# Performance work log

Measured on AMD Instinct MI355X. Metric: run time of the kernel, lower is better.

Reference implementation:

```python
import jax, jax.numpy as jnp
import numpy as np

NUM_HEADS = 8
NUM_LEVELS = 4
NUM_POINTS = 4


def setup_inputs() -> dict:
    key = jax.random.key(0)
    kq, kp, kv, k1, k2, k3, k4 = jax.random.split(key, 7)
    B, Q, C = 4, 4096, 256
    M, L, P = NUM_HEADS, NUM_LEVELS, NUM_POINTS
    shapes_np = np.array([[128, 128], [64, 64], [32, 32], [16, 16]], dtype=np.int32)
    sizes = shapes_np[:, 0] * shapes_np[:, 1]
    N = int(sizes.sum())  # 21760
    level_index = jnp.asarray(np.concatenate([[0], np.cumsum(sizes)[:-1]]).astype(np.int32))
    q = jax.random.normal(kq, (B, Q, C), jnp.float32)
    p = jax.random.uniform(kp, (B, Q, L, 2), jnp.float32)  # normalized ref points
    v = jax.random.normal(kv, (B, N, C), jnp.float32)
    # proj_offset bias: radial grid init from reset_parameters()
    t = np.arange(M, dtype=np.float32) * (2.0 * np.pi / M)
    grid = np.stack([np.cos(t), np.sin(t)], -1)
    grid = grid / np.abs(grid).max(-1, keepdims=True)
    grid = np.tile(grid[:, None, None, :], (1, L, P, 1)) * np.arange(1, P + 1, dtype=np.float32)[None, None, :, None]
    b_off = jnp.asarray(grid.reshape(-1))
    s = 1.0 / np.sqrt(C).astype(np.float32)
    W_off = jax.random.normal(k1, (C, M * L * P * 2), jnp.float32) * 0.01
    W_attn = jax.random.normal(k2, (C, M * L * P), jnp.float32) * s
    b_attn = jnp.zeros((M * L * P,), jnp.float32)
    W_val = jax.random.normal(k3, (C, C), jnp.float32) * s
    b_val = jnp.zeros((C,), jnp.float32)
    W_out = jax.random.normal(k4, (C, C), jnp.float32) * s
    b_out = jnp.zeros((C,), jnp.float32)
    return {"q": q, "p": p, "v": v, "shapes": jnp.asarray(shapes_np), "level_index": level_index,
            "W_off": W_off, "b_off": b_off, "W_attn": W_attn, "b_attn": b_attn,
            "W_val": W_val, "b_val": b_val, "W_out": W_out, "b_out": b_out}


def _ms_deform_attn(q, p, v, shapes, level_index, W_off, b_off, W_attn, b_attn, W_val, b_val, W_out, b_out):
    B, Q, C = q.shape
    M, L, P = NUM_HEADS, NUM_LEVELS, NUM_POINTS
    D = C // M
    N = v.shape[1]
    # value projection -> [B, M, N, D] (head-major for gather)
    v_p = (v @ W_val + b_val).reshape(B, N, M, D).transpose(0, 2, 1, 3)
    # attention weights, softmax over L*P (classic MSDeformAttn kernel contract)
    attn = jax.nn.softmax((q @ W_attn + b_attn).reshape(B, Q, M, L * P), axis=-1)
    attn = attn.reshape(B, Q, M, L, P)
    # sampling locations (P==2 reference-point branch)
    off = (q @ W_off + b_off).reshape(B, Q, M, L, P, 2)
    norm = jnp.stack([shapes[:, 1], shapes[:, 0]], -1).astype(jnp.float32)  # (W, H) per level
    loc = p[:, :, None, :, None, :] + off / norm[None, None, None, :, None, :]  # [B,Q,M,L,P,2]

    out = jnp.zeros((B, M, Q, D), jnp.float32)
    for l in range(L):
        Hf = shapes[l, 0].astype(jnp.float32)
        Wf = shapes[l, 1].astype(jnp.float32)
        Hi = shapes[l, 0]
        Wi = shapes[l, 1]
        base = level_index[l]
        # grid_sample(align_corners=False) convention: pixel = loc*size - 0.5
        x = loc[:, :, :, l, :, 0] * Wf - 0.5  # [B,Q,M,P]
        y = loc[:, :, :, l, :, 1] * Hf - 0.5
        x0 = jnp.floor(x)
        y0 = jnp.floor(y)
        lx, ly = x - x0, y - y0
        x0i = x0.astype(jnp.int32)
        y0i = y0.astype(jnp.int32)

        def corner(xi, yi, w):
            valid = (xi >= 0) & (xi < Wi) & (yi >= 0) & (yi < Hi)
            idx = base + jnp.clip(yi, 0, Hi - 1) * Wi + jnp.clip(xi, 0, Wi - 1)  # [B,Q,M,P]
            idx = idx.transpose(0, 2, 1, 3).reshape(B, M, Q * P)
            g = jnp.take_along_axis(v_p, idx[..., None], axis=2).reshape(B, M, Q, P, D)
            wv = (w * valid.astype(w.dtype)).transpose(0, 2, 1, 3)[..., None]  # [B,M,Q,P,1]
            return g * wv

        samp = (corner(x0i, y0i, (1 - lx) * (1 - ly))
                + corner(x0i + 1, y0i, lx * (1 - ly))
                + corner(x0i, y0i + 1, (1 - lx) * ly)
                + corner(x0i + 1, y0i + 1, lx * ly))  # [B,M,Q,P,D]
        a_l = attn[:, :, :, l, :].transpose(0, 2, 1, 3)  # [B,M,Q,P]
        out = out + jnp.einsum('bmqpd,bmqp->bmqd', samp, a_l)

    out = out.transpose(0, 2, 1, 3).reshape(B, Q, M * D)
    return out @ W_out + b_out


def reference(q, p, v, shapes, level_index, W_off, b_off, W_attn, b_attn, W_val, b_val, W_out, b_out):
    return _ms_deform_attn(q, p, v, shapes, level_index, W_off, b_off, W_attn, b_attn, W_val, b_val, W_out, b_out)
```

## Files before the change

### kernel.cpp

```cpp
#include <hip/hip_runtime.h>
#include <cstddef>

#define BB 4
#define QQ 4096
#define MM 8
#define NN 21760

typedef __bf16 bf16_8 __attribute__((ext_vector_type(8)));
typedef __bf16 bf16_4 __attribute__((ext_vector_type(4)));
typedef float  floatx4 __attribute__((ext_vector_type(4)));

__global__ __launch_bounds__(256) void prep_weights(
    const float* __restrict__ Wv, const float* __restrict__ Wa,
    const float* __restrict__ Wo, const float* __restrict__ Wu,
    const float* __restrict__ ba, const float* __restrict__ bo,
    __bf16* __restrict__ Wt, float* __restrict__ biasq)
{
    const int gid = blockIdx.x * 256 + threadIdx.x;
    if (gid < 65536) {
        const int n = gid >> 8, k = gid & 255;
        Wt[gid] = (__bf16)Wv[k * 256 + n];
    } else if (gid < 163840) {
        const int o = gid - 65536;
        const int n = o >> 8, k = o & 255;
        Wt[gid] = (__bf16)(n < 128 ? Wa[k * 128 + n] : Wo[k * 256 + (n - 128)]);
    } else if (gid < 229376) {
        const int o = gid - 163840;
        const int n = o >> 8, k = o & 255;
        Wt[gid] = (__bf16)Wu[k * 256 + n];
    } else if (gid < 229760) {
        const int j = gid - 229376;
        biasq[j] = (j < 128) ? ba[j] : bo[j - 128];
    }
}

template<typename AT, int NCB, int MODE>
__global__ __launch_bounds__(512, 4) void gemm_ws(
    const AT* __restrict__ A,
    const __bf16* __restrict__ Wn,
    const float* __restrict__ bias,
    void* __restrict__ Cout,
    int tokens, int ldc)
{
    constexpr int F  = NCB / 8;
    constexpr int NJ = F / 16;

    const int z    = blockIdx.z;
    const int col0 = blockIdx.x * NCB;
    const AT* Ab   = A + (size_t)z * tokens * 256;
    const __bf16* Wb = Wn + (size_t)col0 * 256;

    __shared__ __bf16 As[64][256];

    const int tid  = threadIdx.x;
    const int lane = tid & 63;
    const int wave = tid >> 6;
    const int quad = lane >> 4;
    const int l16  = lane & 15;
    const int wave_f = wave * F;

    bf16_8 wf[8][NJ];
    #pragma unroll
    for (int kk = 0; kk < 8; ++kk)
        #pragma unroll
        for (int j = 0; j < NJ; ++j)
            wf[kk][j] = *(const bf16_8*)(Wb + (size_t)(wave_f + j * 16 + l16) * 256
                                          + kk * 32 + quad * 8);

    const int token0 = blockIdx.y * 64;
    if (sizeof(AT) == 4) {
        const float* Af = (const float*)Ab;
        #pragma unroll
        for (int c = 0; c < 8; ++c) {
            const int cid = c * 512 + tid;
            const int r   = cid >> 6;
            const int kc  = (cid & 63) * 4;
            const float4 av = *(const float4*)(Af + (size_t)(token0 + r) * 256 + kc);
            bf16_4 w;
            w[0] = (__bf16)av.x; w[1] = (__bf16)av.y;
            w[2] = (__bf16)av.z; w[3] = (__bf16)av.w;
            const int col = ((((kc >> 3) ^ (r & 7)) << 3) | (kc & 7));
            *(bf16_4*)&As[r][col] = w;
        }
    } else {
        const __bf16* Ah = (const __bf16*)Ab;
        #pragma unroll
        for (int c = 0; c < 4; ++c) {
            const int cid = c * 512 + tid;
            const int r   = cid >> 5;
            const int kc  = (cid & 31) * 8;
            const bf16_8 av = *(const bf16_8*)(Ah + (size_t)(token0 + r) * 256 + kc);
            const int col = (((kc >> 3) ^ (r & 7)) << 3);
            *(bf16_8*)&As[r][col] = av;
        }
    }
    __syncthreads();

    floatx4 acc[NJ][4] = {};
    #pragma unroll
    for (int kk = 0; kk < 8; ++kk) {
        bf16_8 af[4];
        #pragma unroll
        for (int it = 0; it < 4; ++it)
            af[it] = *(const bf16_8*)&As[it * 16 + l16]
                                       [(((kk * 4 + quad) ^ (l16 & 7)) << 3)];
        #pragma unroll
        for (int j = 0; j < NJ; ++j)
            #pragma unroll
            for (int it = 0; it < 4; ++it)
                acc[j][it] = __builtin_amdgcn_mfma_f32_16x16x32_bf16(wf[kk][j], af[it], acc[j][it], 0, 0, 0);
    }

    #pragma unroll
    for (int j = 0; j < NJ; ++j) {
        const int n0 = col0 + wave_f + j * 16 + quad * 4;
        const float4 b4 = *(const float4*)(bias + n0);
        #pragma unroll
        for (int it = 0; it < 4; ++it) {
            const int token = token0 + it * 16 + l16;
            const float v0 = acc[j][it][0] + b4.x;
            const float v1 = acc[j][it][1] + b4.y;
            const float v2 = acc[j][it][2] + b4.z;
            const float v3 = acc[j][it][3] + b4.w;
            if (MODE == 0) {
                float4 o; o.x = v0; o.y = v1; o.z = v2; o.w = v3;
                *(float4*)((float*)Cout + ((size_t)z * tokens + token) * ldc + n0) = o;
            } else {
                const int mh = n0 >> 5, dd = n0 & 31;
                bf16_4 ob;
                ob[0] = (__bf16)v0; ob[1] = (__bf16)v1; ob[2] = (__bf16)v2; ob[3] = (__bf16)v3;
                *(bf16_4*)((__bf16*)Cout + (((size_t)z * 8 + mh) * NN + token) * 32 + dd) = ob;
            }
        }
    }
}

__device__ __forceinline__ float bflo(unsigned u) { return __uint_as_float(u << 16); }
__device__ __forceinline__ float bfhi(unsigned u) { return __uint_as_float(u & 0xffff0000u); }

__global__ __launch_bounds__(512) void sampler(
    const __bf16* __restrict__ vp,
    const float* __restrict__ gqp,
    const float* __restrict__ pref,
    __bf16* __restrict__ mid)
{
    const int t    = threadIdx.x;
    const int m    = t >> 6;
    const int lane = t & 63;
    const int s    = lane >> 2;
    const int c    = lane & 3;
    const int l    = s >> 2;
    const int bq   = blockIdx.x;
    const int b    = bq >> 12;

    const int   Hi = 128 >> l;
    const float Hf = (float)Hi;
    const int   base = (l == 0) ? 0 : (l == 1) ? 16384 : (l == 2) ? 20480 : 21504;

    const float logit = gqp[(size_t)bq * 384 + m * 16 + s];
    const float e = __expf(logit);
    float sum = e;
    #pragma unroll
    for (int k = 4; k < 64; k <<= 1) sum += __shfl_xor(sum, k, 64);
    const float a = e * __builtin_amdgcn_rcpf(sum);

    const float2 off = *(const float2*)(gqp + (size_t)bq * 384 + 128 + (m * 16 + s) * 2);
    const float2 pr  = *(const float2*)(pref + (size_t)bq * 8 + l * 2);

    const float x = fmaf(pr.x, Hf, off.x - 0.5f);
    const float y = fmaf(pr.y, Hf, off.y - 0.5f);
    const float x0f = floorf(x), y0f = floorf(y);
    const float lx = x - x0f, ly = y - y0f;
    const int x0 = (int)x0f, y0 = (int)y0f;
    const int cx0 = min(max(x0, 0), Hi - 1), cx1 = min(max(x0 + 1, 0), Hi - 1);
    const int cy0 = min(max(y0, 0), Hi - 1), cy1 = min(max(y0 + 1, 0), Hi - 1);
    const bool vx0 = (x0 >= 0) && (x0 < Hi), vx1 = (x0 + 1 >= 0) && (x0 + 1 < Hi);
    const bool vy0 = (y0 >= 0) && (y0 < Hi), vy1 = (y0 + 1 >= 0) && (y0 + 1 < Hi);
    const float w00 = a * (1.f - lx) * (1.f - ly) * ((vx0 && vy0) ? 1.f : 0.f);
    const float w10 = a * lx * (1.f - ly) * ((vx1 && vy0) ? 1.f : 0.f);
    const float w01 = a * (1.f - lx) * ly * ((vx0 && vy1) ? 1.f : 0.f);
    const float w11 = a * lx * ly * ((vx1 && vy1) ? 1.f : 0.f);

    const __bf16* vbase = vp + ((size_t)b * 8 + m) * NN * 32;
    const uint4 u00 = *((const uint4*)(vbase + (size_t)(base + cy0 * Hi + cx0) * 32) + c);
    const uint4 u10 = *((const uint4*)(vbase + (size_t)(base + cy0 * Hi + cx1) * 32) + c);
    const uint4 u01 = *((const uint4*)(vbase + (size_t)(base + cy1 * Hi + cx0) * 32) + c);
    const uint4 u11 = *((const uint4*)(vbase + (size_t)(base + cy1 * Hi + cx1) * 32) + c);

    float f[8];
    f[0] = w00*bflo(u00.x) + w10*bflo(u10.x) + w01*bflo(u01.x) + w11*bflo(u11.x);
    f[1] = w00*bfhi(u00.x) + w10*bfhi(u10.x) + w01*bfhi(u01.x) + w11*bfhi(u11.x);
    f[2] = w00*bflo(u00.y) + w10*bflo(u10.y) + w01*bflo(u01.y) + w11*bflo(u11.y);
    f[3] = w00*bfhi(u00.y) + w10*bfhi(u10.y) + w01*bfhi(u01.y) + w11*bfhi(u11.y);
    f[4] = w00*bflo(u00.z) + w10*bflo(u10.z) + w01*bflo(u01.z) + w11*bflo(u11.z);
    f[5] = w00*bfhi(u00.z) + w10*bfhi(u10.z) + w01*bfhi(u01.z) + w11*bfhi(u11.z);
    f[6] = w00*bflo(u00.w) + w10*bflo(u10.w) + w01*bflo(u01.w) + w11*bflo(u11.w);
    f[7] = w00*bfhi(u00.w) + w10*bfhi(u10.w) + w01*bfhi(u01.w) + w11*bfhi(u11.w);

    const int b2 = (lane >> 2) & 1, b3 = (lane >> 3) & 1, b4i = (lane >> 4) & 1;
    #pragma unroll
    for (int j = 0; j < 4; ++j) {
        const float sel  = b2 ? f[j] : f[j + 4];
        const float recv = __shfl_xor(sel, 4, 64);
        f[j] = (b2 ? f[j + 4] : f[j]) + recv;
    }
    #pragma unroll
    for (int j = 0; j < 2; ++j) {
        const float sel  = b3 ? f[j] : f[j + 2];
        const float recv = __shfl_xor(sel, 8, 64);
        f[j] = (b3 ? f[j + 2] : f[j]) + recv;
    }
    {
        const float sel  = b4i ? f[0] : f[1];
        const float recv = __shfl_xor(sel, 16, 64);
        f[0] = (b4i ? f[1] : f[0]) + recv;
    }
    f[0] += __shfl_xor(f[0], 32, 64);

    if (!(lane & 32)) {
        const int chan = (c << 3) | (b2 << 2) | (b3 << 1) | b4i;
        mid[(size_t)bq * 256 + m * 32 + chan] = (__bf16)f[0];
    }
}

extern "C" void kernel_launch(void* const* d_in, const int* in_sizes, int n_in,
                              void* d_out, int out_size, void* d_ws, size_t ws_size,
                              hipStream_t stream) {
    const float* q      = (const float*)d_in[0];
    const float* p      = (const float*)d_in[1];
    const float* v      = (const float*)d_in[2];
    const float* W_off  = (const float*)d_in[5];
    const float* b_off  = (const float*)d_in[6];
    const float* W_attn = (const float*)d_in[7];
    const float* b_attn = (const float*)d_in[8];
    const float* W_val  = (const float*)d_in[9];
    const float* b_val  = (const float*)d_in[10];
    const float* W_out  = (const float*)d_in[11];
    const float* b_out  = (const float*)d_in[12];
    float* out = (float*)d_out;

    float*  gqp   = (float*)d_ws;
    float*  biasq = gqp + (size_t)16384 * 384;
    __bf16* mid   = (__bf16*)(biasq + 384);
    __bf16* vpb   = mid + (size_t)16384 * 256;
    __bf16* Wt    = vpb + (size_t)BB * 8 * NN * 32;
    __bf16* Wt_val = Wt;
    __bf16* Wt_q   = Wt + 65536;
    __bf16* Wt_out = Wt + 163840;

    prep_weights<<<898, 256, 0, stream>>>(W_val, W_attn, W_off, W_out, b_attn, b_off, Wt, biasq);

    {
        dim3 grid(1, 340, BB);
        gemm_ws<float, 256, 1><<<grid, 512, 0, stream>>>(v, Wt_val, b_val, vpb, NN, 0);
    }
    {
        dim3 grid(3, 256, 1);
        gemm_ws<float, 128, 0><<<grid, 512, 0, stream>>>(q, Wt_q, biasq, gqp, BB * QQ, 384);
    }
    sampler<<<BB * QQ, 512, 0, stream>>>(vpb, gqp, p, mid);
    {
        dim3 grid(2, 256, 1);
        gemm_ws<__bf16, 128, 0><<<grid, 512, 0, stream>>>(mid, Wt_out, b_out, out, BB * QQ, 256);
    }
}
```

Baseline: 246.6 us.

## Fuse value and query projection GEMMs into one launch with async LDS loads

Replaces the separate value-projection and query-projection GEMM launches with a single kernel whose flat block index selects the q or v work. Each block handles 32 tokens and stages fp32 activations directly into LDS via global_load_lds, converting to bf16 at fragment load time. The remaining gemm_ws now issues its weight-fragment loads after the A-tile loads. The intent is to cut a launch, improve load balance and overlap global loads, at the cost of smaller tiles, which reload weights more often per token, and twice as much LDS per row for fp32 staging.

```diff
diff --git a/kernel.cpp b/kernel.cpp
--- a/kernel.cpp
+++ b/kernel.cpp
@@ -34,6 +34,128 @@
     }
 }
 
+__global__ __launch_bounds__(512, 4) void gemm_vq2(
+    const float* __restrict__ v,
+    const float* __restrict__ q,
+    const __bf16* __restrict__ Wt,
+    const float* __restrict__ b_val,
+    const float* __restrict__ biasq,
+    __bf16* __restrict__ vpb,
+    float* __restrict__ gqp)
+{
+    __shared__ float Asf[32][256];
+
+    const int tid  = threadIdx.x;
+    const int lane = tid & 63;
+    const int wave = tid >> 6;
+    const int quad = lane >> 4;
+    const int l16  = lane & 15;
+    const int flat = blockIdx.x;
+
+    const float* Arow;
+    const __bf16* Wpan;
+    int tok0, colbase, z = 0;
+    bool is_vp, two;
+    if (flat < 512) {
+        Arow = q;  Wpan = Wt + 65536;
+        tok0 = flat * 32;  colbase = wave * 32;
+        is_vp = false;  two = true;
+    } else if (flat < 1024) {
+        Arow = q;  Wpan = Wt + 65536;
+        tok0 = (flat - 512) * 32;  colbase = 256 + wave * 16;
+        is_vp = false;  two = false;
+    } else {
+        const int f2 = flat - 1024;
+        z = f2 / 680;
+        tok0 = (f2 - z * 680) * 32;
+        Arow = v + (size_t)z * NN * 256;  Wpan = Wt;
+        colbase = wave * 32;
+        is_vp = true;  two = true;
+    }
+
+    #pragma unroll
+    for (int j = 0; j < 4; ++j) {
+        const int r = wave * 4 + j;
+        const float* gp = Arow + (size_t)(tok0 + r) * 256 + ((lane ^ (r & 7)) << 2);
+        __builtin_amdgcn_global_load_lds(
+            (const __attribute__((address_space(1))) void*)gp,
+            (__attribute__((address_space(3))) void*)&Asf[r][0],
+            16, 0, 0);
+    }
+
+    bf16_8 wf[8][2];
+    #pragma unroll
+    for (int kk = 0; kk < 8; ++kk) {
+        wf[kk][0] = *(const bf16_8*)(Wpan + (size_t)(colbase + l16) * 256 + kk * 32 + quad * 8);
+        if (two)
+            wf[kk][1] = *(const bf16_8*)(Wpan + (size_t)(colbase + 16 + l16) * 256 + kk * 32 + quad * 8);
+    }
+
+    __syncthreads();
+
+    floatx4 acc[2][2] = {};
+    #pragma unroll
+    for (int kk = 0; kk < 8; ++kk) {
+        bf16_8 af[2];
+        #pragma unroll
+        for (int it = 0; it < 2; ++it) {
+            const int rr = it * 16 + l16;
+            const int sw = rr & 7;
+            const int c0 = kk * 8 + quad * 2;
+            const float4 x0 = *(const float4*)&Asf[rr][((c0 ^ sw) << 2)];
+            const float4 x1 = *(const float4*)&Asf[rr][(((c0 + 1) ^ sw) << 2)];
+            bf16_8 t;
+            t[0] = (__bf16)x0.x; t[1] = (__bf16)x0.y;
+            t[2] = (__bf16)x0.z; t[3] = (__bf16)x0.w;
+            t[4] = (__bf16)x1.x; t[5] = (__bf16)x1.y;
+            t[6] = (__bf16)x1.z; t[7] = (__bf16)x1.w;
+            af[it] = t;
+        }
+        #pragma unroll
+        for (int it = 0; it < 2; ++it) {
+            acc[0][it] = __builtin_amdgcn_mfma_f32_16x16x32_bf16(wf[kk][0], af[it], acc[0][it], 0, 0, 0);
+            if (two)
+                acc[1][it] = __builtin_amdgcn_mfma_f32_16x16x32_bf16(wf[kk][1], af[it], acc[1][it], 0, 0, 0);
+        }
+    }
+
+    if (is_vp) {
+        #pragma unroll
+        for (int j = 0; j < 2; ++j) {
+            const int n0 = colbase + j * 16 + quad * 4;
+            const float4 b4 = *(const float4*)(b_val + n0);
+            const int mh = n0 >> 5, dd = n0 & 31;
+            #pragma unroll
+            for (int it = 0; it < 2; ++it) {
+                const int token = tok0 + it * 16 + l16;
+                bf16_4 ob;
+                ob[0] = (__bf16)(acc[j][it][0] + b4.x);
+                ob[1] = (__bf16)(acc[j][it][1] + b4.y);
+                ob[2] = (__bf16)(acc[j][it][2] + b4.z);
+                ob[3] = (__bf16)(acc[j][it][3] + b4.w);
+                *(bf16_4*)(vpb + (((size_t)z * 8 + mh) * NN + token) * 32 + dd) = ob;
+            }
+        }
+    } else {
+        #pragma unroll
+        for (int j = 0; j < 2; ++j) {
+            if (j == 1 && !two) break;
+            const int n0 = colbase + j * 16 + quad * 4;
+            const float4 b4 = *(const float4*)(biasq + n0);
+            #pragma unroll
+            for (int it = 0; it < 2; ++it) {
+                const int token = tok0 + it * 16 + l16;
+                float4 ot;
+                ot.x = acc[j][it][0] + b4.x;
+                ot.y = acc[j][it][1] + b4.y;
+                ot.z = acc[j][it][2] + b4.z;
+                ot.w = acc[j][it][3] + b4.w;
+                *(float4*)(gqp + (size_t)token * 384 + n0) = ot;
+            }
+        }
+    }
+}
+
 template<typename AT, int NCB, int MODE>
 __global__ __launch_bounds__(512, 4) void gemm_ws(
     const AT* __restrict__ A,
@@ -59,14 +181,6 @@
     const int l16  = lane & 15;
     const int wave_f = wave * F;
 
-    bf16_8 wf[8][NJ];
-    #pragma unroll
-    for (int kk = 0; kk < 8; ++kk)
-        #pragma unroll
-        for (int j = 0; j < NJ; ++j)
-            wf[kk][j] = *(const bf16_8*)(Wb + (size_t)(wave_f + j * 16 + l16) * 256
-                                          + kk * 32 + quad * 8);
-
     const int token0 = blockIdx.y * 64;
     if (sizeof(AT) == 4) {
         const float* Af = (const float*)Ab;
@@ -94,6 +208,14 @@
             *(bf16_8*)&As[r][col] = av;
         }
     }
+
+    bf16_8 wf[8][NJ];
+    #pragma unroll
+    for (int kk = 0; kk < 8; ++kk)
+        #pragma unroll
+        for (int j = 0; j < NJ; ++j)
+            wf[kk][j] = *(const bf16_8*)(Wb + (size_t)(wave_f + j * 16 + l16) * 256
+                                          + kk * 32 + quad * 8);
     __syncthreads();
 
     floatx4 acc[NJ][4] = {};
@@ -244,21 +366,14 @@
     __bf16* mid   = (__bf16*)(biasq + 384);
     __bf16* vpb   = mid + (size_t)16384 * 256;
     __bf16* Wt    = vpb + (size_t)BB * 8 * NN * 32;
-    __bf16* Wt_val = Wt;
-    __bf16* Wt_q   = Wt + 65536;
     __bf16* Wt_out = Wt + 163840;
 
     prep_weights<<<898, 256, 0, stream>>>(W_val, W_attn, W_off, W_out, b_attn, b_off, Wt, biasq);
 
-    {
-        dim3 grid(1, 340, BB);
-        gemm_ws<float, 256, 1><<<grid, 512, 0, stream>>>(v, Wt_val, b_val, vpb, NN, 0);
-    }
-    {
-        dim3 grid(3, 256, 1);
-        gemm_ws<float, 128, 0><<<grid, 512, 0, stream>>>(q, Wt_q, biasq, gqp, BB * QQ, 384);
-    }
+    gemm_vq2<<<3744, 512, 0, stream>>>(v, q, Wt, b_val, biasq, vpb, gqp);
+
     sampler<<<BB * QQ, 512, 0, stream>>>(vpb, gqp, p, mid);
+
     {
         dim3 grid(2, 256, 1);
         gemm_ws<__bf16, 128, 0><<<grid, 512, 0, stream>>>(mid, Wt_out, b_out, out, BB * QQ, 256);
```

Result: slower. 266.2 us (+7.9%).

## Merge value and query projection GEMMs into one pipelined double-buffered kernel

Applied to the files above, without the earlier changes.

Replaces the two separate projection launches (value projection and query offset/attention projection) with a single kernel whose blocks are split by index between the two jobs. Each block processes two 64-token tiles in K-halves, using a double-buffered shared-memory A tile and register prefetch so global loads overlap the MFMA work. It also moves the weight-fragment loads in the remaining GEMM after the A staging loads so their latency overlaps. The cost is branchy per-block role dispatch, a leftover dead weight-load loop, and more complex indexing.

```diff
diff --git a/kernel.cpp b/kernel.cpp
--- a/kernel.cpp
+++ b/kernel.cpp
@@ -34,6 +34,164 @@
     }
 }
 
+__global__ __launch_bounds__(512, 4) void gemm_vq4(
+    const float* __restrict__ v,
+    const float* __restrict__ q,
+    const __bf16* __restrict__ Wt,
+    const float* __restrict__ b_val,
+    const float* __restrict__ biasq,
+    __bf16* __restrict__ vpb,
+    float* __restrict__ gqp)
+{
+    __shared__ __bf16 As[2][64][128];
+
+    const int tid  = threadIdx.x;
+    const int lane = tid & 63;
+    const int wave = tid >> 6;
+    const int quad = lane >> 4;
+    const int l16  = lane & 15;
+    const int flat = blockIdx.x;
+
+    const bool is_vp = (flat >= 384);
+    int z = 0, tb, colep;
+    const float* Arow;
+    const __bf16* Wpan;
+    if (is_vp) {
+        const int bi = flat - 384;
+        z  = bi / 170;
+        tb = (bi - z * 170) * 128;
+        Arow  = v + (size_t)z * NN * 256;
+        Wpan  = Wt;
+        colep = wave * 32;
+    } else {
+        const int g0 = flat * 2;
+        const int slice = g0 >> 8;
+        tb = (g0 & 255) * 64;
+        Arow  = q;
+        Wpan  = Wt + 65536 + (size_t)(slice * 128) * 256;
+        colep = slice * 128 + wave * 16;
+    }
+
+    float4 a4[4];
+    auto issue = [&](int ph) {
+        const int tile = ph >> 1, h = ph & 1;
+        #pragma unroll
+        for (int c = 0; c < 4; ++c) {
+            const int cid = c * 512 + tid;
+            const int rr  = cid >> 5;
+            const int kc  = (cid & 31) * 4;
+            a4[c] = *(const float4*)(Arow + (size_t)(tb + tile * 64 + rr) * 256
+                                      + h * 128 + kc);
+        }
+    };
+    auto wr = [&](int ph) {
+        const int buf = ph & 1;
+        #pragma unroll
+        for (int c = 0; c < 4; ++c) {
+            const int cid = c * 512 + tid;
+            const int rr  = cid >> 5;
+            const int kc  = (cid & 31) * 4;
+            bf16_4 w;
+            w[0] = (__bf16)a4[c].x; w[1] = (__bf16)a4[c].y;
+            w[2] = (__bf16)a4[c].z; w[3] = (__bf16)a4[c].w;
+            const int col = ((((kc >> 3) ^ (rr & 7)) << 3) | (kc & 7));
+            *(bf16_4*)&As[buf][rr][col] = w;
+        }
+    };
+
+    issue(0);
+
+    bf16_8 wf0[8], wf1[8];
+    #pragma unroll
+    for (int kk = 0; kk < 8; ++kk) {
+        wf0[kk] = *(const bf16_8*)(Wpan + (size_t)(colep % 384 - (is_vp ? 0 : (colep - wave * 16 - (colep >= 128 ? (colep >= 256 ? 256 : 128) : 0))) * 0 + 0) * 0
+                                    + 0);
+    }
+    {
+        const int wrow0 = is_vp ? (wave * 32) : (wave * 16);
+        #pragma unroll
+        for (int kk = 0; kk < 8; ++kk) {
+            wf0[kk] = *(const bf16_8*)(Wpan + (size_t)(wrow0 + l16) * 256 + kk * 32 + quad * 8);
+            if (is_vp)
+                wf1[kk] = *(const bf16_8*)(Wpan + (size_t)(wrow0 + 16 + l16) * 256 + kk * 32 + quad * 8);
+        }
+    }
+
+    wr(0);
+    issue(1);
+    asm volatile("s_waitcnt lgkmcnt(0)" ::: "memory");
+    __builtin_amdgcn_s_barrier();
+
+    floatx4 acc0[4], acc1[4];
+    #pragma unroll
+    for (int p = 0; p < 4; ++p) {
+        if ((p & 1) == 0) {
+            #pragma unroll
+            for (int it = 0; it < 4; ++it) { acc0[it] = (floatx4){0,0,0,0}; acc1[it] = (floatx4){0,0,0,0}; }
+        }
+        {
+            const int buf = p & 1, h = p & 1;
+            #pragma unroll
+            for (int k2 = 0; k2 < 4; ++k2) {
+                const int kk = h * 4 + k2;
+                bf16_8 af[4];
+                #pragma unroll
+                for (int it = 0; it < 4; ++it)
+                    af[it] = *(const bf16_8*)&As[buf][it * 16 + l16]
+                                               [(((k2 * 4 + quad) ^ (l16 & 7)) << 3)];
+                #pragma unroll
+                for (int it = 0; it < 4; ++it) {
+                    acc0[it] = __builtin_amdgcn_mfma_f32_16x16x32_bf16(wf0[kk], af[it], acc0[it], 0, 0, 0);
+                    if (is_vp)
+                        acc1[it] = __builtin_amdgcn_mfma_f32_16x16x32_bf16(wf1[kk], af[it], acc1[it], 0, 0, 0);
+                }
+            }
+        }
+        if (p & 1) {
+            const int tile = p >> 1;
+            const int tok0 = tb + tile * 64;
+            if (is_vp) {
+                #pragma unroll
+                for (int j = 0; j < 2; ++j) {
+                    const int n0 = colep + j * 16 + quad * 4;
+                    const float4 b4 = *(const float4*)(b_val + n0);
+                    const int mh = n0 >> 5, dd = n0 & 31;
+                    #pragma unroll
+                    for (int it = 0; it < 4; ++it) {
+                        const int token = tok0 + it * 16 + l16;
+                        const floatx4 av = j ? acc1[it] : acc0[it];
+                        bf16_4 ob;
+                        ob[0] = (__bf16)(av[0] + b4.x);
+                        ob[1] = (__bf16)(av[1] + b4.y);
+                        ob[2] = (__bf16)(av[2] + b4.z);
+                        ob[3] = (__bf16)(av[3] + b4.w);
+                        *(bf16_4*)(vpb + (((size_t)z * 8 + mh) * NN + token) * 32 + dd) = ob;
+                    }
+                }
+            } else {
+                const int n0 = colep + quad * 4;
+                const float4 b4 = *(const float4*)(biasq + n0);
+                #pragma unroll
+                for (int it = 0; it < 4; ++it) {
+                    const int token = tok0 + it * 16 + l16;
+                    float4 ot;
+                    ot.x = acc0[it][0] + b4.x;
+                    ot.y = acc0[it][1] + b4.y;
+                    ot.z = acc0[it][2] + b4.z;
+                    ot.w = acc0[it][3] + b4.w;
+                    *(float4*)(gqp + (size_t)token * 384 + n0) = ot;
+                }
+            }
+        }
+        if (p < 3) {
+            wr(p + 1);
+            if (p < 2) issue(p + 2);
+            asm volatile("s_waitcnt lgkmcnt(0)" ::: "memory");
+            __builtin_amdgcn_s_barrier();
+        }
+    }
+}
+
 template<typename AT, int NCB, int MODE>
 __global__ __launch_bounds__(512, 4) void gemm_ws(
     const AT* __restrict__ A,
@@ -59,14 +217,6 @@
     const int l16  = lane & 15;
     const int wave_f = wave * F;
 
-    bf16_8 wf[8][NJ];
-    #pragma unroll
-    for (int kk = 0; kk < 8; ++kk)
-        #pragma unroll
-        for (int j = 0; j < NJ; ++j)
-            wf[kk][j] = *(const bf16_8*)(Wb + (size_t)(wave_f + j * 16 + l16) * 256
-                                          + kk * 32 + quad * 8);
-
     const int token0 = blockIdx.y * 64;
     if (sizeof(AT) == 4) {
         const float* Af = (const float*)Ab;
@@ -94,6 +244,14 @@
             *(bf16_8*)&As[r][col] = av;
         }
     }
+
+    bf16_8 wf[8][NJ];
+    #pragma unroll
+    for (int kk = 0; kk < 8; ++kk)
+        #pragma unroll
+        for (int j = 0; j < NJ; ++j)
+            wf[kk][j] = *(const bf16_8*)(Wb + (size_t)(wave_f + j * 16 + l16) * 256
+                                          + kk * 32 + quad * 8);
     __syncthreads();
 
     floatx4 acc[NJ][4] = {};
@@ -244,21 +402,14 @@
     __bf16* mid   = (__bf16*)(biasq + 384);
     __bf16* vpb   = mid + (size_t)16384 * 256;
     __bf16* Wt    = vpb + (size_t)BB * 8 * NN * 32;
-    __bf16* Wt_val = Wt;
-    __bf16* Wt_q   = Wt + 65536;
     __bf16* Wt_out = Wt + 163840;
 
     prep_weights<<<898, 256, 0, stream>>>(W_val, W_attn, W_off, W_out, b_attn, b_off, Wt, biasq);
 
-    {
-        dim3 grid(1, 340, BB);
-        gemm_ws<float, 256, 1><<<grid, 512, 0, stream>>>(v, Wt_val, b_val, vpb, NN, 0);
-    }
-    {
-        dim3 grid(3, 256, 1);
-        gemm_ws<float, 128, 0><<<grid, 512, 0, stream>>>(q, Wt_q, biasq, gqp, BB * QQ, 384);
-    }
+    gemm_vq4<<<1064, 512, 0, stream>>>(v, q, Wt, b_val, biasq, vpb, gqp);
+
     sampler<<<BB * QQ, 512, 0, stream>>>(vpb, gqp, p, mid);
+
     {
         dim3 grid(2, 256, 1);
         gemm_ws<__bf16, 128, 0><<<grid, 512, 0, stream>>>(mid, Wt_out, b_out, out, BB * QQ, 256);
```

Measured after the change: 296.2 us. +20.1%, slower.
